# Kernel tuning notes

Hardware: AMD Instinct MI355X
Metric: run time of the kernel (lower is better)

The kernel has to match this reference:

```python
import jax, jax.numpy as jnp
import numpy as np

S, B, N, K, D, H = 4, 8, 2048, 16, 32, 128


def setup_inputs() -> dict:
    key = jax.random.key(0)
    ks = jax.random.split(key, 7)
    x = jax.random.normal(ks[0], (S, B, N, D), dtype=jnp.float32)
    mu = jax.random.normal(ks[1], (S, B, K, D), dtype=jnp.float32)
    tau = jax.random.uniform(ks[2], (S, B, K, D), dtype=jnp.float32)  # precisions > 0
    # Linear(3D -> H); stored as (3D, H) i.e. transpose of torch's (H, 3D) weight
    W1 = jax.random.normal(ks[3], (3 * D, H), dtype=jnp.float32) * (1.0 / np.sqrt(3 * D))
    b1 = jax.random.normal(ks[4], (H,), dtype=jnp.float32) * 0.01
    W2 = jax.random.normal(ks[5], (H, 1), dtype=jnp.float32) * (1.0 / np.sqrt(H))
    b2 = jax.random.normal(ks[6], (1,), dtype=jnp.float32) * 0.01
    return {"x": x, "mu": mu, "tau": tau, "W1": W1, "b1": b1, "W2": W2, "b2": b2}


def reference(x, mu, tau, W1, b1, W2, b2):
    # Original torch code materializes var = cat([x_expand, mu_expand, tau_expand], -1)
    # of shape (S,B,N,K,3D) then applies Linear(3D,H). Mathematically identical:
    # split W1 rows into the x / mu / tau blocks and add the partial projections,
    # which avoids building the (S,B,N,K,3D) concat tensor.
    d = x.shape[-1]
    Wx, Wm, Wt = W1[:d], W1[d:2 * d], W1[2 * d:]
    hx = jnp.einsum('sbnd,dh->sbnh', x, Wx)                       # (S,B,N,H)
    hk = jnp.einsum('sbkd,dh->sbkh', mu, Wm) \
       + jnp.einsum('sbkd,dh->sbkh', tau, Wt)                     # (S,B,K,H)
    h = jnp.tanh(hx[:, :, :, None, :] + hk[:, :, None, :, :] + b1)  # (S,B,N,K,H)
    gamma = jnp.einsum('sbnkh,h->sbnk', h, W2[:, 0]) + b2[0]        # (S,B,N,K)
    q_probs = jax.nn.softmax(gamma, axis=-1)
    return q_probs
```

## Files before the change

kernel.cpp:

```cpp
#include <hip/hip_runtime.h>
#include <math.h>

#define EXP2F(x) __builtin_amdgcn_exp2f(x)
#define RCPF(x)  __builtin_amdgcn_rcpf(x)
#define C_SCALE 2.8853900817779268f
#define L2E 1.4426950408889634f

typedef __attribute__((address_space(4))) const float c4f;
static __device__ __forceinline__ c4f* as_const(const float* p) {
  return (c4f*)(unsigned long long)p;
}

__global__ __launch_bounds__(256) void prep_kernel(
    const float* __restrict__ mu, const float* __restrict__ tau,
    const float* __restrict__ W1, const float* __restrict__ b1,
    const float* __restrict__ W2,
    float* __restrict__ ekT, float* __restrict__ WTc, float* __restrict__ w2n) {
  int g = blockIdx.x * 256 + threadIdx.x;
  int k = g & 15, h = (g >> 4) & 127, sb = g >> 11;
  int row = sb * 16 + k;
  const float* mur  = mu  + row * 32;
  const float* taur = tau + row * 32;
  float acc = b1[h];
#pragma unroll
  for (int d = 0; d < 32; ++d) {
    acc = fmaf(mur[d],  W1[(32 + d) * 128 + h], acc);
    acc = fmaf(taur[d], W1[(64 + d) * 128 + h], acc);
  }
  ekT[g] = EXP2F(C_SCALE * acc);
  if (g < 4096) {
    int hh = g >> 5, d = g & 31;
    WTc[g] = C_SCALE * W1[d * 128 + hh];
  }
  if (g < 128) w2n[g] = -2.0f * W2[g];
}

__global__ __launch_bounds__(256, 4) void main_kernel(
    const float* __restrict__ x, const float* __restrict__ WTc,
    const float* __restrict__ ekT, const float* __restrict__ w2n,
    float* __restrict__ out) {
  __shared__ float pSum[4][64][17];
  int t = threadIdx.x;
  int lane = t & 63;
  int wv = __builtin_amdgcn_readfirstlane(t >> 6);
  int row0 = blockIdx.x * 64;
  int sb = row0 >> 11;
  int r = row0 + lane;

  float xr[32];
  {
    const float4* xp = (const float4*)(x + (size_t)r * 32);
#pragma unroll
    for (int i = 0; i < 8; ++i) {
      float4 v = xp[i];
      xr[4 * i] = v.x; xr[4 * i + 1] = v.y; xr[4 * i + 2] = v.z; xr[4 * i + 3] = v.w;
    }
  }

  c4f* Wb  = as_const(WTc + wv * 32 * 32);
  c4f* ekb = as_const(ekT + (size_t)sb * 2048 + wv * 32 * 16);
  c4f* w2b = as_const(w2n + wv * 32);

  float acc[16];
#pragma unroll
  for (int k = 0; k < 16; ++k) acc[k] = 0.f;

#pragma unroll 1
  for (int hh = 0; hh < 32; ++hh) {
    c4f* wr = Wb + hh * 32;
    float d0 = 0.f, d1 = 0.f, d2 = 0.f, d3 = 0.f;
#pragma unroll
    for (int i = 0; i < 8; ++i) {
      d0 = fmaf(xr[4 * i],     wr[4 * i],     d0);
      d1 = fmaf(xr[4 * i + 1], wr[4 * i + 1], d1);
      d2 = fmaf(xr[4 * i + 2], wr[4 * i + 2], d2);
      d3 = fmaf(xr[4 * i + 3], wr[4 * i + 3], d3);
    }
    float ex = EXP2F((d0 + d1) + (d2 + d3));
    c4f* ekr = ekb + hh * 16;
    float w2 = w2b[hh];
#pragma unroll
    for (int k = 0; k < 16; ++k) {
      float tt = fmaf(ex, ekr[k], 1.0f);
      acc[k] = fmaf(w2, RCPF(tt), acc[k]);
    }
  }

#pragma unroll
  for (int k = 0; k < 16; ++k) pSum[wv][lane][k] = acc[k];
  __syncthreads();

  int rr = t >> 2, q = t & 3;
  int kb = q * 4;
  float g0 = pSum[0][rr][kb]     + pSum[1][rr][kb]     + pSum[2][rr][kb]     + pSum[3][rr][kb];
  float g1 = pSum[0][rr][kb + 1] + pSum[1][rr][kb + 1] + pSum[2][rr][kb + 1] + pSum[3][rr][kb + 1];
  float g2 = pSum[0][rr][kb + 2] + pSum[1][rr][kb + 2] + pSum[2][rr][kb + 2] + pSum[3][rr][kb + 2];
  float g3 = pSum[0][rr][kb + 3] + pSum[1][rr][kb + 3] + pSum[2][rr][kb + 3] + pSum[3][rr][kb + 3];

  float mx = fmaxf(fmaxf(g0, g1), fmaxf(g2, g3));
#pragma unroll
  for (int m = 1; m <= 2; m <<= 1) mx = fmaxf(mx, __shfl_xor(mx, m, 4));
  float p0 = EXP2F((g0 - mx) * L2E), p1 = EXP2F((g1 - mx) * L2E);
  float p2 = EXP2F((g2 - mx) * L2E), p3 = EXP2F((g3 - mx) * L2E);
  float sum = (p0 + p1) + (p2 + p3);
#pragma unroll
  for (int m = 1; m <= 2; m <<= 1) sum += __shfl_xor(sum, m, 4);
  float inv = RCPF(sum);
  float4 o = {p0 * inv, p1 * inv, p2 * inv, p3 * inv};
  *(float4*)&out[(size_t)(row0 + rr) * 16 + q * 4] = o;
}

extern "C" void kernel_launch(void* const* d_in, const int* in_sizes, int n_in,
                              void* d_out, int out_size, void* d_ws, size_t ws_size,
                              hipStream_t stream) {
  const float* x   = (const float*)d_in[0];
  const float* mu  = (const float*)d_in[1];
  const float* tau = (const float*)d_in[2];
  const float* W1  = (const float*)d_in[3];
  const float* b1  = (const float*)d_in[4];
  const float* W2  = (const float*)d_in[5];
  float* out = (float*)d_out;

  float* ekT = (float*)d_ws;
  float* WTc = ekT + 32 * 2048;
  float* w2n = WTc + 4096;
  (void)in_sizes; (void)n_in; (void)out_size; (void)ws_size;

  prep_kernel<<<256, 256, 0, stream>>>(mu, tau, W1, b1, W2, ekT, WTc, w2n);
  main_kernel<<<1024, 256, 0, stream>>>(x, WTc, ekT, w2n, out);
}
```

Baseline: 100.1 us.

## Use packed FMA, paired reciprocals, and split hidden dim across 8 waves

```diff
diff --git a/kernel.cpp b/kernel.cpp
--- a/kernel.cpp
+++ b/kernel.cpp
@@ -1,10 +1,20 @@
 #include <hip/hip_runtime.h>
 #include <math.h>
+
+typedef float v2f __attribute__((ext_vector_type(2)));
 
 #define EXP2F(x) __builtin_amdgcn_exp2f(x)
 #define RCPF(x)  __builtin_amdgcn_rcpf(x)
 #define C_SCALE 2.8853900817779268f
 #define L2E 1.4426950408889634f
+
+static __device__ __forceinline__ v2f fma2(v2f a, v2f b, v2f c) {
+#if __has_builtin(__builtin_elementwise_fma)
+  return __builtin_elementwise_fma(a, b, c);
+#else
+  v2f r; r.x = fmaf(a.x, b.x, c.x); r.y = fmaf(a.y, b.y, c.y); return r;
+#endif
+}
 
 typedef __attribute__((address_space(4))) const float c4f;
 static __device__ __forceinline__ c4f* as_const(const float* p) {
@@ -35,11 +45,11 @@
   if (g < 128) w2n[g] = -2.0f * W2[g];
 }
 
-__global__ __launch_bounds__(256, 4) void main_kernel(
+__global__ __launch_bounds__(512, 8) void main_kernel(
     const float* __restrict__ x, const float* __restrict__ WTc,
     const float* __restrict__ ekT, const float* __restrict__ w2n,
     float* __restrict__ out) {
-  __shared__ float pSum[4][64][17];
+  __shared__ float pSum[8][64][18];
   int t = threadIdx.x;
   int lane = t & 63;
   int wv = __builtin_amdgcn_readfirstlane(t >> 6);
@@ -47,67 +57,72 @@
   int sb = row0 >> 11;
   int r = row0 + lane;
 
-  float xr[32];
+  v2f xr[16];
   {
     const float4* xp = (const float4*)(x + (size_t)r * 32);
 #pragma unroll
     for (int i = 0; i < 8; ++i) {
       float4 v = xp[i];
-      xr[4 * i] = v.x; xr[4 * i + 1] = v.y; xr[4 * i + 2] = v.z; xr[4 * i + 3] = v.w;
+      xr[2 * i]     = (v2f){v.x, v.y};
+      xr[2 * i + 1] = (v2f){v.z, v.w};
     }
   }
 
-  c4f* Wb  = as_const(WTc + wv * 32 * 32);
-  c4f* ekb = as_const(ekT + (size_t)sb * 2048 + wv * 32 * 16);
-  c4f* w2b = as_const(w2n + wv * 32);
+  c4f* Wb  = as_const(WTc + wv * 16 * 32);
+  c4f* ekb = as_const(ekT + (size_t)sb * 2048 + wv * 16 * 16);
+  c4f* w2b = as_const(w2n + wv * 16);
 
-  float acc[16];
+  v2f acc[8];
 #pragma unroll
-  for (int k = 0; k < 16; ++k) acc[k] = 0.f;
+  for (int j = 0; j < 8; ++j) acc[j] = (v2f){0.f, 0.f};
 
 #pragma unroll 1
-  for (int hh = 0; hh < 32; ++hh) {
+  for (int hh = 0; hh < 16; ++hh) {
     c4f* wr = Wb + hh * 32;
-    float d0 = 0.f, d1 = 0.f, d2 = 0.f, d3 = 0.f;
+    v2f p = (v2f){0.f, 0.f};
 #pragma unroll
-    for (int i = 0; i < 8; ++i) {
-      d0 = fmaf(xr[4 * i],     wr[4 * i],     d0);
-      d1 = fmaf(xr[4 * i + 1], wr[4 * i + 1], d1);
-      d2 = fmaf(xr[4 * i + 2], wr[4 * i + 2], d2);
-      d3 = fmaf(xr[4 * i + 3], wr[4 * i + 3], d3);
+    for (int i = 0; i < 16; ++i) {
+      v2f w = (v2f){wr[2 * i], wr[2 * i + 1]};
+      p = fma2(xr[i], w, p);
     }
-    float ex = EXP2F((d0 + d1) + (d2 + d3));
+    float ex = EXP2F(p.x + p.y);
     c4f* ekr = ekb + hh * 16;
     float w2 = w2b[hh];
+    v2f ex2 = (v2f){ex, ex};
+    v2f w22 = (v2f){w2, w2};
 #pragma unroll
-    for (int k = 0; k < 16; ++k) {
-      float tt = fmaf(ex, ekr[k], 1.0f);
-      acc[k] = fmaf(w2, RCPF(tt), acc[k]);
+    for (int j = 0; j < 8; ++j) {
+      v2f ek2 = (v2f){ekr[2 * j], ekr[2 * j + 1]};
+      v2f tt = fma2(ex2, ek2, (v2f){1.f, 1.f});
+      float pr = tt.x * tt.y;
+      float rc = RCPF(pr);
+      v2f inv = (v2f){tt.y * rc, tt.x * rc};
+      acc[j] = fma2(w22, inv, acc[j]);
     }
   }
 
 #pragma unroll
-  for (int k = 0; k < 16; ++k) pSum[wv][lane][k] = acc[k];
+  for (int j = 0; j < 8; ++j)
+    *(v2f*)&pSum[wv][lane][2 * j] = acc[j];
   __syncthreads();
 
-  int rr = t >> 2, q = t & 3;
-  int kb = q * 4;
-  float g0 = pSum[0][rr][kb]     + pSum[1][rr][kb]     + pSum[2][rr][kb]     + pSum[3][rr][kb];
-  float g1 = pSum[0][rr][kb + 1] + pSum[1][rr][kb + 1] + pSum[2][rr][kb + 1] + pSum[3][rr][kb + 1];
-  float g2 = pSum[0][rr][kb + 2] + pSum[1][rr][kb + 2] + pSum[2][rr][kb + 2] + pSum[3][rr][kb + 2];
-  float g3 = pSum[0][rr][kb + 3] + pSum[1][rr][kb + 3] + pSum[2][rr][kb + 3] + pSum[3][rr][kb + 3];
+  int rr = t >> 3, kp = t & 7;
+  v2f g = (v2f){0.f, 0.f};
+#pragma unroll
+  for (int w = 0; w < 8; ++w) {
+    v2f v = *(const v2f*)&pSum[w][rr][2 * kp];
+    g.x += v.x; g.y += v.y;
+  }
 
-  float mx = fmaxf(fmaxf(g0, g1), fmaxf(g2, g3));
+  float mx = fmaxf(g.x, g.y);
 #pragma unroll
-  for (int m = 1; m <= 2; m <<= 1) mx = fmaxf(mx, __shfl_xor(mx, m, 4));
-  float p0 = EXP2F((g0 - mx) * L2E), p1 = EXP2F((g1 - mx) * L2E);
-  float p2 = EXP2F((g2 - mx) * L2E), p3 = EXP2F((g3 - mx) * L2E);
-  float sum = (p0 + p1) + (p2 + p3);
+  for (int m = 1; m <= 4; m <<= 1) mx = fmaxf(mx, __shfl_xor(mx, m, 8));
+  float p0 = EXP2F((g.x - mx) * L2E), p1 = EXP2F((g.y - mx) * L2E);
+  float sum = p0 + p1;
 #pragma unroll
-  for (int m = 1; m <= 2; m <<= 1) sum += __shfl_xor(sum, m, 4);
+  for (int m = 1; m <= 4; m <<= 1) sum += __shfl_xor(sum, m, 8);
   float inv = RCPF(sum);
-  float4 o = {p0 * inv, p1 * inv, p2 * inv, p3 * inv};
-  *(float4*)&out[(size_t)(row0 + rr) * 16 + q * 4] = o;
+  *(float2*)&out[(size_t)(row0 + rr) * 16 + 2 * kp] = make_float2(p0 * inv, p1 * inv);
 }
 
 extern "C" void kernel_launch(void* const* d_in, const int* in_sizes, int n_in,
@@ -127,5 +142,5 @@
   (void)in_sizes; (void)n_in; (void)out_size; (void)ws_size;
 
   prep_kernel<<<256, 256, 0, stream>>>(mu, tau, W1, b1, W2, ekT, WTc, w2n);
-  main_kernel<<<1024, 256, 0, stream>>>(x, WTc, ekT, w2n, out);
+  main_kernel<<<1024, 512, 0, stream>>>(x, WTc, ekT, w2n, out);
 }
```

Measured after the change: 95.79 us. 4.3% less time.
